# Kernel tuning notes

Hardware: AMD Instinct MI355X
Metric: run time of the kernel (lower is better)

## Reference

```python
import jax, jax.numpy as jnp
import numpy as np

V, E, H, C = 50257, 256, 512, 16  # vocab, embed_dim, hidden_size, n_cells
B, T = 256, 128
LN_EPS = 1e-5


def setup_inputs() -> dict:
    key = jax.random.key(0)
    ks = jax.random.split(key, 16)
    s_h = 1.0 / np.sqrt(H)
    s_e = 1.0 / np.sqrt(E)
    return {
        "tokens": jax.random.randint(ks[0], (B, T), 0, V),
        "emb": jax.random.normal(ks[1], (V, E), jnp.float32) * 0.02,
        "Wproj": jax.random.normal(ks[2], (E, H), jnp.float32) * s_e,
        "bproj": jnp.zeros((H,), jnp.float32),
        "Wp": jax.random.normal(ks[3], (C, H, H), jnp.float32) * s_h,
        "bp": jnp.zeros((C, H), jnp.float32),
        "ln_g": jnp.ones((C, H), jnp.float32),
        "ln_b": jnp.zeros((C, H), jnp.float32),
        "Wih": jax.random.normal(ks[4], (C, 4 * H, H), jnp.float32) * s_h,
        "bih": jnp.zeros((C, 4 * H), jnp.float32),
        "Whh": jax.random.normal(ks[5], (C, 4 * H, H), jnp.float32) * s_h,
        "bhh": jnp.zeros((C, 4 * H), jnp.float32),
        "Wa": jax.random.normal(ks[6], (C, H, H), jnp.float32) * s_h,
        "ba": jnp.zeros((C, H), jnp.float32),
        "gate_logit": jnp.zeros((C,), jnp.float32),  # torch.tensor(0.0) per cell
    }


def _layernorm(x, g, b):
    mu = jnp.mean(x, axis=-1, keepdims=True)
    var = jnp.var(x, axis=-1, keepdims=True)
    return (x - mu) * jax.lax.rsqrt(var + LN_EPS) * g + b


def reference(tokens, emb, Wproj, bproj, Wp, bp, ln_g, ln_b,
              Wih, bih, Whh, bhh, Wa, ba, gate_logit):
    # embedding (padding_idx=0 zeroed) + projection to hidden size
    emb = emb.at[0].set(0.0)
    xs = emb[tokens] @ Wproj + bproj              # [B,T,H]
    xs = jnp.transpose(xs, (1, 0, 2))             # [T,B,H] for scan

    gate = jax.nn.sigmoid(gate_logit)[:, None, None]  # [C,1,1]

    def step(carry, x_t):
        h, c, ext = carry                          # h,c: [C,B,H], ext: [B,H]
        # input_adapter == Identity (input_size == hidden_size); external injection
        x = x_t[None] + 0.3 * ext[None]            # [C,B,H]
        # perception: Linear + ReLU + LayerNorm
        p = jax.nn.relu(jnp.einsum('cbh,chk->cbk', x, Wp) + bp[:, None, :])
        p = _layernorm(p, ln_g[:, None, :], ln_b[:, None, :])
        # LSTMCell (torch gate order i, f, g, o)
        gates = (jnp.einsum('cbh,cgh->cbg', p, Wih) + bih[:, None, :]
                 + jnp.einsum('cbh,cgh->cbg', h, Whh) + bhh[:, None, :])
        i_g, f_g, g_g, o_g = jnp.split(gates, 4, axis=-1)
        c_new = jax.nn.sigmoid(f_g) * c + jax.nn.sigmoid(i_g) * jnp.tanh(g_g)
        h_new = jax.nn.sigmoid(o_g) * jnp.tanh(c_new)
        # association + sigmoid gate
        a = jnp.tanh(jnp.einsum('cbh,chk->cbk', h_new, Wa) + ba[:, None, :])
        out = a * gate                             # [C,B,H]
        y = jnp.mean(out, axis=0)                  # aggregate cells -> [B,H]
        return (h_new, c_new, y), y

    h0 = jnp.zeros((C, B, H), xs.dtype)
    c0 = jnp.zeros((C, B, H), xs.dtype)
    ext0 = jnp.zeros((B, H), xs.dtype)
    _, ys = jax.lax.scan(step, (h0, c0, ext0), xs)  # ys: [T,B,H]
    return jnp.transpose(ys, (1, 0, 2))             # [B,T,H]
```

## Files before the change

### kernel.cpp

```cpp
#include <hip/hip_runtime.h>
#include <hip/hip_bf16.h>

#define V 50257
#define E 256
#define H 512
#define C 16
#define B 256
#define T 128

typedef _Float16 f16x8 __attribute__((ext_vector_type(8)));
typedef _Float16 f16x4 __attribute__((ext_vector_type(4)));
typedef float f32x4 __attribute__((ext_vector_type(4)));

__device__ __forceinline__ float sigm(float x) { return 1.0f / (1.0f + __expf(-x)); }

__device__ __forceinline__ void gload16(const _Float16* g, _Float16* l) {
  __builtin_amdgcn_global_load_lds((const __attribute__((address_space(1))) unsigned*)g,
                                   (__attribute__((address_space(3))) unsigned*)l, 16, 0, 0);
}

__global__ __launch_bounds__(256) void k_emb(const int* __restrict__ tokens,
                                             const float* __restrict__ emb,
                                             const float* __restrict__ Wproj,
                                             const float* __restrict__ bproj,
                                             _Float16* __restrict__ xs_h) {
  __shared__ float elds[16][256];
  const int tid = threadIdx.x;
  const int r0 = blockIdx.x * 16;
#pragma unroll
  for (int i = 0; i < 16; ++i) {
    int r = r0 + i;
    int t = r >> 8, b = r & 255;
    int tok = tokens[b * T + t];
    elds[i][tid] = (tok == 0) ? 0.0f : emb[(size_t)tok * E + tid];
  }
  __syncthreads();
  float acc0[16], acc1[16];
#pragma unroll
  for (int i = 0; i < 16; ++i) { acc0[i] = 0.0f; acc1[i] = 0.0f; }
  for (int k = 0; k < E; k += 4) {
    float w0[4], w1[4];
#pragma unroll
    for (int kk = 0; kk < 4; ++kk) {
      w0[kk] = Wproj[(k + kk) * H + tid];
      w1[kk] = Wproj[(k + kk) * H + tid + 256];
    }
#pragma unroll
    for (int i = 0; i < 16; ++i) {
      float4 e4 = *(const float4*)&elds[i][k];
      acc0[i] = fmaf(e4.x, w0[0], acc0[i]);
      acc0[i] = fmaf(e4.y, w0[1], acc0[i]);
      acc0[i] = fmaf(e4.z, w0[2], acc0[i]);
      acc0[i] = fmaf(e4.w, w0[3], acc0[i]);
      acc1[i] = fmaf(e4.x, w1[0], acc1[i]);
      acc1[i] = fmaf(e4.y, w1[1], acc1[i]);
      acc1[i] = fmaf(e4.z, w1[2], acc1[i]);
      acc1[i] = fmaf(e4.w, w1[3], acc1[i]);
    }
  }
  float bp0 = bproj[tid], bp1 = bproj[tid + 256];
#pragma unroll
  for (int i = 0; i < 16; ++i) {
    size_t r = (size_t)(r0 + i);
    xs_h[r * H + tid] = (_Float16)(acc0[i] + bp0);
    xs_h[r * H + tid + 256] = (_Float16)(acc1[i] + bp1);
  }
}

__global__ __launch_bounds__(256) void k_cvt_wg(const float* __restrict__ Wih,
                                                const float* __restrict__ Whh,
                                                _Float16* __restrict__ WgT) {
  for (size_t i4 = ((size_t)blockIdx.x * 256 + threadIdx.x) * 4; i4 < (size_t)33554432;
       i4 += (size_t)gridDim.x * 1024) {
    size_t c = i4 >> 21;
    size_t rem = i4 & 2097151;
    size_t np = rem >> 10;
    size_t k2 = rem & 1023;
    int gate = (int)((np >> 4) & 3);
    int hh = (int)(((np >> 6) << 4) | (np & 15));
    size_t n = (size_t)gate * 512 + hh;
    const float* src = (k2 < 512) ? (Wih + (c * 2048 + n) * 512 + k2)
                                  : (Whh + (c * 2048 + n) * 512 + (k2 - 512));
    float4 v = *(const float4*)src;
    f16x4 o;
    o[0] = (_Float16)v.x; o[1] = (_Float16)v.y; o[2] = (_Float16)v.z; o[3] = (_Float16)v.w;
    *(f16x4*)&WgT[i4] = o;
  }
}

__global__ __launch_bounds__(256) void k_cvt_tr(const float* __restrict__ W,
                                                _Float16* __restrict__ WT) {
  __shared__ float tl[64][65];
  const int tid = threadIdx.x;
  const int c = blockIdx.z;
  const int k0 = blockIdx.y * 64, n0 = blockIdx.x * 64;
  const float* Wc = W + (size_t)c * 262144;
#pragma unroll
  for (int q = 0; q < 16; ++q) {
    int idx = q * 256 + tid;
    int r = idx >> 6, cc = idx & 63;
    tl[r][cc] = Wc[(size_t)(k0 + r) * 512 + n0 + cc];
  }
  __syncthreads();
  _Float16* WTc = WT + (size_t)c * 262144;
#pragma unroll
  for (int q = 0; q < 16; ++q) {
    int idx = q * 256 + tid;
    int rr = idx >> 6, cc = idx & 63;
    WTc[(size_t)(n0 + rr) * 512 + k0 + cc] = (_Float16)tl[cc][rr];
  }
}

__global__ __launch_bounds__(256) void k_bias(const float* __restrict__ bih,
                                              const float* __restrict__ bhh,
                                              float* __restrict__ bsum) {
  int i = blockIdx.x * 256 + threadIdx.x;
  if (i < C * 4 * H) {
    int c = i >> 11, np = i & 2047;
    int gate = (np >> 4) & 3;
    int hh = ((np >> 6) << 4) | (np & 15);
    int n = gate * 512 + hh;
    bsum[i] = bih[c * 2048 + n] + bhh[c * 2048 + n];
  }
}

__global__ __launch_bounds__(256, 2) void k_pln(const _Float16* __restrict__ xq,
                                                const _Float16* __restrict__ WpT,
                                                const float* __restrict__ bp,
                                                const float* __restrict__ ln_g,
                                                const float* __restrict__ ln_b,
                                                _Float16* __restrict__ Pdst) {
  __shared__ _Float16 Bsl[512 * 64];
  const int tid = threadIdx.x;
  const int w = tid >> 6, l = tid & 63;
  const int blk = blockIdx.x;
  const int c = blk & 15;
  const int mt = blk >> 4;
  const int m0 = mt * 32;
  const _Float16* Bb = WpT + (size_t)c * 262144;
  const int srow = l >> 3, sj = l & 7;
  const int lm = l & 15, lk = l >> 4;
  f32x4 acc[2][8];
#pragma unroll
  for (int i = 0; i < 2; ++i)
#pragma unroll
    for (int j = 0; j < 8; ++j) acc[i][j] = (f32x4)0.0f;
  const _Float16* pA0 = xq + (size_t)(m0 + lm) * 512 + lk * 8;
  const _Float16* pA1 = pA0 + 16 * 512;
  f16x8 a0s0 = *(const f16x8*)pA0;
  f16x8 a0s1 = *(const f16x8*)(pA0 + 32);
  f16x8 a1s0 = *(const f16x8*)pA1;
  f16x8 a1s1 = *(const f16x8*)(pA1 + 32);
#pragma unroll 1
  for (int kb = 0; kb < 8; ++kb) {
#pragma unroll
    for (int q = 0; q < 16; ++q) {
      int r = q * 32 + w * 8 + srow;
      int gj = sj ^ (r & 7);
      gload16(Bb + (size_t)r * 512 + kb * 64 + gj * 8, &Bsl[(q * 32 + w * 8) * 64]);
    }
    f16x8 u00 = a0s0, u01 = a0s1, u10 = a1s0, u11 = a1s1;
    if (kb < 7) {
      a0s0 = *(const f16x8*)(pA0 + (kb + 1) * 64);
      a0s1 = *(const f16x8*)(pA0 + (kb + 1) * 64 + 32);
      a1s0 = *(const f16x8*)(pA1 + (kb + 1) * 64);
      a1s1 = *(const f16x8*)(pA1 + (kb + 1) * 64 + 32);
    }
    __syncthreads();
#pragma unroll
    for (int s2 = 0; s2 < 2; ++s2) {
      f16x8 bf[8];
#pragma unroll
      for (int j = 0; j < 8; ++j) {
        int RN = w * 128 + j * 16 + lm;
        int pn = (s2 * 4 + lk) ^ (RN & 7);
        bf[j] = *(const f16x8*)&Bsl[RN * 64 + pn * 8];
      }
      f16x8 ua = s2 ? u01 : u00;
      f16x8 ub = s2 ? u11 : u10;
#pragma unroll
      for (int j = 0; j < 8; ++j) {
        acc[0][j] = __builtin_amdgcn_mfma_f32_16x16x32_f16(ua, bf[j], acc[0][j], 0, 0, 0);
        acc[1][j] = __builtin_amdgcn_mfma_f32_16x16x32_f16(ub, bf[j], acc[1][j], 0, 0, 0);
      }
    }
    __syncthreads();
  }
  float bv[8], gcol[8], bcol[8];
#pragma unroll
  for (int j = 0; j < 8; ++j) {
    int col = w * 128 + j * 16 + lm;
    bv[j] = bp[c * 512 + col];
    gcol[j] = ln_g[c * 512 + col];
    bcol[j] = ln_b[c * 512 + col];
  }
  float vals[2][8][4];
  float s1l[2][4], s2l[2][4];
#pragma unroll
  for (int i = 0; i < 2; ++i)
#pragma unroll
    for (int rg = 0; rg < 4; ++rg) { s1l[i][rg] = 0.0f; s2l[i][rg] = 0.0f; }
#pragma unroll
  for (int i = 0; i < 2; ++i)
#pragma unroll
    for (int j = 0; j < 8; ++j)
#pragma unroll
      for (int rg = 0; rg < 4; ++rg) {
        float v = fmaxf(acc[i][j][rg] + bv[j], 0.0f);
        vals[i][j][rg] = v;
        s1l[i][rg] += v;
        s2l[i][rg] += v * v;
      }
#pragma unroll
  for (int m = 1; m < 16; m <<= 1) {
#pragma unroll
    for (int i = 0; i < 2; ++i)
#pragma unroll
      for (int rg = 0; rg < 4; ++rg) {
        s1l[i][rg] += __shfl_xor(s1l[i][rg], m, 64);
        s2l[i][rg] += __shfl_xor(s2l[i][rg], m, 64);
      }
  }
  float* st = (float*)Bsl;
  if (lm == 0) {
#pragma unroll
    for (int i = 0; i < 2; ++i)
#pragma unroll
      for (int rg = 0; rg < 4; ++rg) {
        int row = i * 16 + lk * 4 + rg;
        st[(w * 32 + row) * 2] = s1l[i][rg];
        st[(w * 32 + row) * 2 + 1] = s2l[i][rg];
      }
  }
  __syncthreads();
  float mu_[2][4], rs_[2][4];
#pragma unroll
  for (int i = 0; i < 2; ++i)
#pragma unroll
    for (int rg = 0; rg < 4; ++rg) {
      int row = i * 16 + lk * 4 + rg;
      float t1 = 0.0f, t2 = 0.0f;
#pragma unroll
      for (int ww = 0; ww < 4; ++ww) {
        t1 += st[(ww * 32 + row) * 2];
        t2 += st[(ww * 32 + row) * 2 + 1];
      }
      float mu = t1 * (1.0f / 512.0f);
      float var = t2 * (1.0f / 512.0f) - mu * mu;
      mu_[i][rg] = mu;
      rs_[i][rg] = rsqrtf(var + 1e-5f);
    }
#pragma unroll
  for (int i = 0; i < 2; ++i)
#pragma unroll
    for (int j = 0; j < 8; ++j) {
      int col = w * 128 + j * 16 + lm;
#pragma unroll
      for (int rg = 0; rg < 4; ++rg) {
        int row = i * 16 + lk * 4 + rg;
        float o = (vals[i][j][rg] - mu_[i][rg]) * rs_[i][rg] * gcol[j] + bcol[j];
        Pdst[((size_t)c * 256 + m0 + row) * 1024 + col] = (_Float16)o;
      }
    }
}

__global__ __launch_bounds__(256, 2) void k_gates(const _Float16* __restrict__ A,
                                                  const _Float16* __restrict__ Bm,
                                                  const float* __restrict__ bias,
                                                  float* __restrict__ cstate,
                                                  _Float16* __restrict__ hdst) {
  __shared__ _Float16 sm[2 * 20480];
  const int tid = threadIdx.x;
  const int w = tid >> 6, l = tid & 63;
  const int blk = blockIdx.x;
  const int c = blk & 15;
  const int n0 = (blk >> 4) * 64;
  const _Float16* Ab = A + (size_t)c * 262144;
  const _Float16* Bb = Bm + (size_t)c * 2097152 + (size_t)n0 * 1024;
  f32x4 acc[4][4];
#pragma unroll
  for (int i = 0; i < 4; ++i)
#pragma unroll
    for (int j = 0; j < 4; ++j) acc[i][j] = (f32x4)0.0f;
  const int wm = w * 64;
  const int srow = l >> 3, sj = l & 7;
  const int lm = l & 15, lk = l >> 4;

  auto STAGE = [&](int buf, int kb) {
    _Float16* As = sm + buf * 20480;
    _Float16* Bs = As + 16384;
#pragma unroll
    for (int q = 0; q < 8; ++q) {
      int rb = q * 32 + w * 8;
      int r = rb + srow;
      int gj = sj ^ (r & 7);
      gload16(Ab + (size_t)r * 1024 + kb * 64 + gj * 8, &As[rb * 64]);
    }
#pragma unroll
    for (int q = 0; q < 2; ++q) {
      int rb = q * 32 + w * 8;
      int r = rb + srow;
      int gj = sj ^ (r & 7);
      gload16(Bb + (size_t)r * 1024 + kb * 64 + gj * 8, &Bs[rb * 64]);
    }
  };

  STAGE(0, 0);
#pragma unroll 1
  for (int kb = 0; kb < 16; ++kb) {
    const int cur = kb & 1;
    if (kb < 15) {
      STAGE(cur ^ 1, kb + 1);
      asm volatile("s_waitcnt vmcnt(10)" ::: "memory");
    } else {
      asm volatile("s_waitcnt vmcnt(0)" ::: "memory");
    }
    __builtin_amdgcn_s_barrier();
    __builtin_amdgcn_sched_barrier(0);
    const _Float16* As = sm + cur * 20480;
    const _Float16* Bs = As + 16384;
#pragma unroll
    for (int s2 = 0; s2 < 2; ++s2) {
      f16x8 af[4], bf[4];
#pragma unroll
      for (int i = 0; i < 4; ++i) {
        int R = wm + i * 16 + lm;
        int p = (s2 * 4 + lk) ^ (R & 7);
        af[i] = *(const f16x8*)&As[R * 64 + p * 8];
        int RN = i * 16 + lm;
        int pn = (s2 * 4 + lk) ^ (RN & 7);
        bf[i] = *(const f16x8*)&Bs[RN * 64 + pn * 8];
      }
#pragma unroll
      for (int i = 0; i < 4; ++i)
#pragma unroll
        for (int j = 0; j < 4; ++j)
          acc[i][j] = __builtin_amdgcn_mfma_f32_16x16x32_f16(af[i], bf[j], acc[i][j], 0, 0, 0);
    }
    asm volatile("s_waitcnt lgkmcnt(0)" ::: "memory");
    __builtin_amdgcn_s_barrier();
  }
  const int rl = lk * 4, cl = lm;
  const int hh = ((n0 >> 6) << 4) + cl;
  float bv[4];
#pragma unroll
  for (int j = 0; j < 4; ++j) bv[j] = bias[(size_t)c * 2048 + n0 + j * 16 + cl];
#pragma unroll
  for (int i = 0; i < 4; ++i) {
#pragma unroll
    for (int rg = 0; rg < 4; ++rg) {
      int row = wm + i * 16 + rl + rg;
      float ig = acc[i][0][rg] + bv[0];
      float fg = acc[i][1][rg] + bv[1];
      float gg = acc[i][2][rg] + bv[2];
      float og = acc[i][3][rg] + bv[3];
      size_t ci = ((size_t)c * 256 + row) * 512 + hh;
      float cn = sigm(fg) * cstate[ci] + sigm(ig) * tanhf(gg);
      cstate[ci] = cn;
      hdst[((size_t)c * 256 + row) * 1024 + 512 + hh] = (_Float16)(sigm(og) * tanhf(cn));
    }
  }
}

__global__ __launch_bounds__(256, 2) void k_assoc(const _Float16* __restrict__ An,
                                                  const _Float16* __restrict__ WaT,
                                                  const float* __restrict__ ba,
                                                  const float* __restrict__ gl,
                                                  _Float16* __restrict__ abuf) {
  __shared__ _Float16 Asl[64 * 64];
  __shared__ _Float16 Bsl[128 * 64];
  const int tid = threadIdx.x;
  const int w = tid >> 6, l = tid & 63;
  const int blk = blockIdx.x;
  const int c = blk & 15;
  const int r_ = blk >> 4;
  const int nt = r_ & 3, mt = r_ >> 2;
  const int n0 = nt * 128;
  const _Float16* Ab = An + 512 + ((size_t)c * 256 + mt * 64) * 1024;
  const _Float16* Bb = WaT + (size_t)c * 262144 + (size_t)n0 * 512;
  f32x4 acc[2][4];
#pragma unroll
  for (int i = 0; i < 2; ++i)
#pragma unroll
    for (int j = 0; j < 4; ++j) acc[i][j] = (f32x4)0.0f;
  const int wm = (w >> 1) * 32, wn = (w & 1) * 64;
  const int srow = l >> 3, sj = l & 7;
  const int lm = l & 15, lk = l >> 4;
#pragma unroll 1
  for (int kb = 0; kb < 8; ++kb) {
#pragma unroll
    for (int q = 0; q < 2; ++q) {
      int r = q * 32 + w * 8 + srow;
      int gj = sj ^ (r & 7);
      gload16(Ab + (size_t)r * 1024 + kb * 64 + gj * 8, &Asl[(q * 32 + w * 8) * 64]);
    }
#pragma unroll
    for (int q = 0; q < 4; ++q) {
      int r = q * 32 + w * 8 + srow;
      int gj = sj ^ (r & 7);
      gload16(Bb + (size_t)r * 512 + kb * 64 + gj * 8, &Bsl[(q * 32 + w * 8) * 64]);
    }
    __syncthreads();
#pragma unroll
    for (int s2 = 0; s2 < 2; ++s2) {
      f16x8 af[2], bf[4];
#pragma unroll
      for (int i = 0; i < 2; ++i) {
        int R = wm + i * 16 + lm;
        int p = (s2 * 4 + lk) ^ (R & 7);
        af[i] = *(const f16x8*)&Asl[R * 64 + p * 8];
      }
#pragma unroll
      for (int j = 0; j < 4; ++j) {
        int RN = wn + j * 16 + lm;
        int pn = (s2 * 4 + lk) ^ (RN & 7);
        bf[j] = *(const f16x8*)&Bsl[RN * 64 + pn * 8];
      }
#pragma unroll
      for (int i = 0; i < 2; ++i)
#pragma unroll
        for (int j = 0; j < 4; ++j)
          acc[i][j] = __builtin_amdgcn_mfma_f32_16x16x32_f16(af[i], bf[j], acc[i][j], 0, 0, 0);
    }
    __syncthreads();
  }
  float gv = sigm(gl[c]);
#pragma unroll
  for (int i = 0; i < 2; ++i)
#pragma unroll
    for (int j = 0; j < 4; ++j) {
      int gc = n0 + wn + j * 16 + lm;
      float bav = ba[c * 512 + gc];
#pragma unroll
      for (int rg = 0; rg < 4; ++rg) {
        int row = mt * 64 + wm + i * 16 + lk * 4 + rg;
        float v = tanhf(acc[i][j][rg] + bav) * gv;
        abuf[(size_t)c * 131072 + (size_t)row * 512 + gc] = (_Float16)v;
      }
    }
}

__global__ __launch_bounds__(256) void k_agg(const _Float16* __restrict__ abuf,
                                             const _Float16* __restrict__ xs_h,
                                             _Float16* __restrict__ xq,
                                             float* __restrict__ out, int t) {
  int idx = blockIdx.x * 256 + threadIdx.x;
  int i4 = idx * 4;
  float s[4] = {0.0f, 0.0f, 0.0f, 0.0f};
#pragma unroll
  for (int c = 0; c < 16; ++c) {
    f16x4 a = *(const f16x4*)&abuf[(size_t)c * 131072 + i4];
#pragma unroll
    for (int j = 0; j < 4; ++j) s[j] += (float)a[j];
  }
  int b = i4 >> 9, h = i4 & 511;
  float4 y4;
  float* yp = &y4.x;
#pragma unroll
  for (int j = 0; j < 4; ++j) yp[j] = s[j] * (1.0f / 16.0f);
  *(float4*)&out[((size_t)b * T + t) * 512 + h] = y4;
  if (t + 1 < T) {
    f16x4 xs4 = *(const f16x4*)&xs_h[(size_t)(t + 1) * 131072 + i4];
    f16x4 xn;
#pragma unroll
    for (int j = 0; j < 4; ++j) xn[j] = (_Float16)((float)xs4[j] + 0.3f * yp[j]);
    *(f16x4*)&xq[i4] = xn;
  }
}

extern "C" void kernel_launch(void* const* d_in, const int* in_sizes, int n_in,
                              void* d_out, int out_size, void* d_ws, size_t ws_size,
                              hipStream_t stream) {
  const int* tokens = (const int*)d_in[0];
  const float* emb = (const float*)d_in[1];
  const float* Wproj = (const float*)d_in[2];
  const float* bproj = (const float*)d_in[3];
  const float* Wp = (const float*)d_in[4];
  const float* bp = (const float*)d_in[5];
  const float* ln_g = (const float*)d_in[6];
  const float* ln_b = (const float*)d_in[7];
  const float* Wih = (const float*)d_in[8];
  const float* bih = (const float*)d_in[9];
  const float* Whh = (const float*)d_in[10];
  const float* bhh = (const float*)d_in[11];
  const float* Wa = (const float*)d_in[12];
  const float* ba = (const float*)d_in[13];
  const float* gl = (const float*)d_in[14];
  float* out = (float*)d_out;

  char* w8 = (char*)d_ws;
  _Float16* xs_h = (_Float16*)w8;
  _Float16* Aq0 = (_Float16*)(w8 + 33554432);
  _Float16* Aq1 = (_Float16*)(w8 + 50331648);
  float* cbuf = (float*)(w8 + 67108864);
  _Float16* abuf = (_Float16*)(w8 + 75497472);
  _Float16* xq = (_Float16*)(w8 + 79691776);
  _Float16* WpT = (_Float16*)(w8 + 79953920);
  _Float16* WaT = (_Float16*)(w8 + 88342528);
  _Float16* WgT = (_Float16*)(w8 + 96731136);
  float* bsum = (float*)(w8 + 163840000);

  hipMemsetAsync(Aq0, 0, 16777216, stream);
  hipMemsetAsync(cbuf, 0, 8388608, stream);

  k_cvt_wg<<<4096, 256, 0, stream>>>(Wih, Whh, WgT);
  k_cvt_tr<<<dim3(8, 8, 16), 256, 0, stream>>>(Wp, WpT);
  k_cvt_tr<<<dim3(8, 8, 16), 256, 0, stream>>>(Wa, WaT);
  k_bias<<<128, 256, 0, stream>>>(bih, bhh, bsum);
  k_emb<<<T * B / 16, 256, 0, stream>>>(tokens, emb, Wproj, bproj, xs_h);
  hipMemcpyAsync(xq, xs_h, 262144, hipMemcpyDeviceToDevice, stream);

  for (int t = 0; t < T; ++t) {
    _Float16* Ac = (t & 1) ? Aq1 : Aq0;
    _Float16* An = (t & 1) ? Aq0 : Aq1;
    k_pln<<<128, 256, 0, stream>>>(xq, WpT, bp, ln_g, ln_b, Ac);
    k_gates<<<512, 256, 0, stream>>>(Ac, WgT, bsum, cbuf, An);
    k_assoc<<<256, 256, 0, stream>>>(An, WaT, ba, gl, abuf);
    k_agg<<<128, 256, 0, stream>>>(abuf, xs_h, xq, out, t);
  }
}
```

Baseline: 7.698 ms.

## Fuse cell aggregation and input mixing into the perception kernel

Removes the per-step aggregation kernel. The perception kernel now reads the 16 cell outputs from the previous step, sums them in fp16, forms the next input x = xs + 0.3*mean, and writes the previous step's output (block group c==0). A final kernel writes the last timestep. This cuts one launch per step plus the xq round trip. In exchange, each of the 16 cell blocks redundantly re-reads the whole abuf slice, the 16-way sum is done in fp16 with lower precision, and register pressure rises from holding all A fragments plus fully unrolling the k loop.

```diff
diff --git a/kernel.cpp b/kernel.cpp
--- a/kernel.cpp
+++ b/kernel.cpp
@@ -124,12 +124,14 @@
   }
 }
 
-__global__ __launch_bounds__(256, 2) void k_pln(const _Float16* __restrict__ xq,
+__global__ __launch_bounds__(256, 2) void k_pln(const _Float16* __restrict__ xs_t,
+                                                const _Float16* __restrict__ abuf,
                                                 const _Float16* __restrict__ WpT,
                                                 const float* __restrict__ bp,
                                                 const float* __restrict__ ln_g,
                                                 const float* __restrict__ ln_b,
-                                                _Float16* __restrict__ Pdst) {
+                                                _Float16* __restrict__ Pdst,
+                                                float* __restrict__ out, int t) {
   __shared__ _Float16 Bsl[512 * 64];
   const int tid = threadIdx.x;
   const int w = tid >> 6, l = tid & 63;
@@ -140,18 +142,49 @@
   const _Float16* Bb = WpT + (size_t)c * 262144;
   const int srow = l >> 3, sj = l & 7;
   const int lm = l & 15, lk = l >> 4;
+
+  f16x8 xreg[2][16];
+  const _Float16 cmix = (_Float16)0.01875f;
+#pragma unroll
+  for (int r = 0; r < 2; ++r) {
+    int row = m0 + r * 16 + lm;
+#pragma unroll
+    for (int q = 0; q < 16; ++q) {
+      int col = (q >> 1) * 64 + (q & 1) * 32 + lk * 8;
+      f16x8 xv = *(const f16x8*)&xs_t[(size_t)row * 512 + col];
+      if (t > 0) {
+        f16x8 av[16];
+#pragma unroll
+        for (int cc = 0; cc < 16; ++cc)
+          av[cc] = *(const f16x8*)&abuf[(size_t)cc * 131072 + (size_t)row * 512 + col];
+#pragma unroll
+        for (int m = 8; m >= 1; m >>= 1)
+#pragma unroll
+          for (int i = 0; i < m; ++i) av[i] = av[i] + av[i + m];
+        f16x8 S = av[0];
+        f16x8 xn;
+#pragma unroll
+        for (int j = 0; j < 8; ++j) xn[j] = xv[j] + cmix * S[j];
+        xreg[r][q] = xn;
+        if (c == 0) {
+          float* op = &out[((size_t)row * T + (t - 1)) * 512 + col];
+          *(float4*)op = make_float4((float)S[0] * 0.0625f, (float)S[1] * 0.0625f,
+                                     (float)S[2] * 0.0625f, (float)S[3] * 0.0625f);
+          *(float4*)(op + 4) = make_float4((float)S[4] * 0.0625f, (float)S[5] * 0.0625f,
+                                           (float)S[6] * 0.0625f, (float)S[7] * 0.0625f);
+        }
+      } else {
+        xreg[r][q] = xv;
+      }
+    }
+  }
+
   f32x4 acc[2][8];
 #pragma unroll
   for (int i = 0; i < 2; ++i)
 #pragma unroll
     for (int j = 0; j < 8; ++j) acc[i][j] = (f32x4)0.0f;
-  const _Float16* pA0 = xq + (size_t)(m0 + lm) * 512 + lk * 8;
-  const _Float16* pA1 = pA0 + 16 * 512;
-  f16x8 a0s0 = *(const f16x8*)pA0;
-  f16x8 a0s1 = *(const f16x8*)(pA0 + 32);
-  f16x8 a1s0 = *(const f16x8*)pA1;
-  f16x8 a1s1 = *(const f16x8*)(pA1 + 32);
-#pragma unroll 1
+#pragma unroll
   for (int kb = 0; kb < 8; ++kb) {
 #pragma unroll
     for (int q = 0; q < 16; ++q) {
@@ -159,13 +192,6 @@
       int gj = sj ^ (r & 7);
       gload16(Bb + (size_t)r * 512 + kb * 64 + gj * 8, &Bsl[(q * 32 + w * 8) * 64]);
     }
-    f16x8 u00 = a0s0, u01 = a0s1, u10 = a1s0, u11 = a1s1;
-    if (kb < 7) {
-      a0s0 = *(const f16x8*)(pA0 + (kb + 1) * 64);
-      a0s1 = *(const f16x8*)(pA0 + (kb + 1) * 64 + 32);
-      a1s0 = *(const f16x8*)(pA1 + (kb + 1) * 64);
-      a1s1 = *(const f16x8*)(pA1 + (kb + 1) * 64 + 32);
-    }
     __syncthreads();
 #pragma unroll
     for (int s2 = 0; s2 < 2; ++s2) {
@@ -176,8 +202,8 @@
         int pn = (s2 * 4 + lk) ^ (RN & 7);
         bf[j] = *(const f16x8*)&Bsl[RN * 64 + pn * 8];
       }
-      f16x8 ua = s2 ? u01 : u00;
-      f16x8 ub = s2 ? u11 : u10;
+      f16x8 ua = xreg[0][kb * 2 + s2];
+      f16x8 ub = xreg[1][kb * 2 + s2];
 #pragma unroll
       for (int j = 0; j < 8; ++j) {
         acc[0][j] = __builtin_amdgcn_mfma_f32_16x16x32_f16(ua, bf[j], acc[0][j], 0, 0, 0);
@@ -440,10 +466,8 @@
     }
 }
 
-__global__ __launch_bounds__(256) void k_agg(const _Float16* __restrict__ abuf,
-                                             const _Float16* __restrict__ xs_h,
-                                             _Float16* __restrict__ xq,
-                                             float* __restrict__ out, int t) {
+__global__ __launch_bounds__(256) void k_fin(const _Float16* __restrict__ abuf,
+                                             float* __restrict__ out) {
   int idx = blockIdx.x * 256 + threadIdx.x;
   int i4 = idx * 4;
   float s[4] = {0.0f, 0.0f, 0.0f, 0.0f};
@@ -455,17 +479,8 @@
   }
   int b = i4 >> 9, h = i4 & 511;
   float4 y4;
-  float* yp = &y4.x;
-#pragma unroll
-  for (int j = 0; j < 4; ++j) yp[j] = s[j] * (1.0f / 16.0f);
-  *(float4*)&out[((size_t)b * T + t) * 512 + h] = y4;
-  if (t + 1 < T) {
-    f16x4 xs4 = *(const f16x4*)&xs_h[(size_t)(t + 1) * 131072 + i4];
-    f16x4 xn;
-#pragma unroll
-    for (int j = 0; j < 4; ++j) xn[j] = (_Float16)((float)xs4[j] + 0.3f * yp[j]);
-    *(f16x4*)&xq[i4] = xn;
-  }
+  y4.x = s[0] * 0.0625f; y4.y = s[1] * 0.0625f; y4.z = s[2] * 0.0625f; y4.w = s[3] * 0.0625f;
+  *(float4*)&out[((size_t)b * T + (T - 1)) * 512 + h] = y4;
 }
 
 extern "C" void kernel_launch(void* const* d_in, const int* in_sizes, int n_in,
@@ -494,7 +509,6 @@
   _Float16* Aq1 = (_Float16*)(w8 + 50331648);
   float* cbuf = (float*)(w8 + 67108864);
   _Float16* abuf = (_Float16*)(w8 + 75497472);
-  _Float16* xq = (_Float16*)(w8 + 79691776);
   _Float16* WpT = (_Float16*)(w8 + 79953920);
   _Float16* WaT = (_Float16*)(w8 + 88342528);
   _Float16* WgT = (_Float16*)(w8 + 96731136);
@@ -508,14 +522,14 @@
   k_cvt_tr<<<dim3(8, 8, 16), 256, 0, stream>>>(Wa, WaT);
   k_bias<<<128, 256, 0, stream>>>(bih, bhh, bsum);
   k_emb<<<T * B / 16, 256, 0, stream>>>(tokens, emb, Wproj, bproj, xs_h);
-  hipMemcpyAsync(xq, xs_h, 262144, hipMemcpyDeviceToDevice, stream);
 
   for (int t = 0; t < T; ++t) {
     _Float16* Ac = (t & 1) ? Aq1 : Aq0;
     _Float16* An = (t & 1) ? Aq0 : Aq1;
-    k_pln<<<128, 256, 0, stream>>>(xq, WpT, bp, ln_g, ln_b, Ac);
+    k_pln<<<128, 256, 0, stream>>>(xs_h + (size_t)t * 131072, abuf, WpT, bp, ln_g, ln_b,
+                                   Ac, out, t);
     k_gates<<<512, 256, 0, stream>>>(Ac, WgT, bsum, cbuf, An);
     k_assoc<<<256, 256, 0, stream>>>(An, WaT, ba, gl, abuf);
-    k_agg<<<128, 256, 0, stream>>>(abuf, xs_h, xq, out, t);
-  }
-}
+  }
+  k_fin<<<128, 256, 0, stream>>>(abuf, out);
+}
```

Result: slower. 14.70 ms (+91.0%).
